# Optimization experiments

Hardware: AMD Instinct MI355X
Metric: run time of the kernel (lower is better)

## Reference

```python
import jax, jax.numpy as jnp
import numpy as np

B = 1024
D = 512
M = 65536          # num_memory
C = 4096           # num pseudo-label clusters (= labels.max()+1, fixed for jit)
TEMP = 0.05
EPS = 1e-6


def setup_inputs() -> dict:
    key = jax.random.key(0)
    k1, k2, k3, k4 = jax.random.split(key, 4)
    inputs = jax.random.normal(k1, (B, D), dtype=jnp.float32)
    indexes = jax.random.randint(k2, (B,), 0, M, dtype=jnp.int64)
    feats = jax.random.normal(k3, (M, D), dtype=jnp.float32)
    # memory bank stores L2-normalized features (see _update_feature)
    features = feats / jnp.linalg.norm(feats, axis=1, keepdims=True)
    labels = jax.random.randint(k4, (M,), 0, C, dtype=jnp.int64)
    return {"inputs": inputs, "indexes": indexes, "features": features, "labels": labels}


def reference(inputs, indexes, features, labels):
    # F.normalize(inputs, p=2, dim=1)
    x = inputs / jnp.linalg.norm(inputs, axis=1, keepdims=True)
    # HM.forward: inputs @ features.T, then / temp  -> sim over memory slots [B, M]
    sim = (x @ features.T) / TEMP
    # index_add over labels: per-cluster sum of sim columns  -> [C, B]
    sim_c = jax.ops.segment_sum(sim.T, labels, num_segments=C)
    nums = jax.ops.segment_sum(jnp.ones((M,), dtype=sim.dtype), labels, num_segments=C)  # [C]
    cluster_mask = (nums > 0).astype(sim.dtype)                     # [C]
    # mean within cluster; empty clusters divide by 1
    avg = sim_c / jnp.where(nums > 0, nums, 1.0)[:, None]           # [C, B]
    # masked_softmax over clusters, per sample
    vec = avg.T                                                     # [B, C]
    masked_exps = jnp.exp(vec) * cluster_mask[None, :]
    probs = masked_exps / (jnp.sum(masked_exps, axis=1, keepdims=True) + EPS)
    # F.nll_loss(log(probs + eps), targets) with targets = labels[indexes]
    targets = labels[indexes]                                       # [B]
    logp = jnp.log(probs + EPS)
    loss = -jnp.mean(logp[jnp.arange(B), targets])
    return loss
```

## Files before the change

kernel.cpp:

```cpp
#include <hip/hip_runtime.h>
#include <hip/hip_bf16.h>

#define NB 1024
#define ND 512
#define NM 65536
#define NC 4096
#define CAP 128

static constexpr float TEMP = 0.05f;
static constexpr float EPSF = 1e-6f;

typedef __attribute__((ext_vector_type(8))) short short8v;
typedef __attribute__((ext_vector_type(16))) float f32x16;

static __device__ __forceinline__ short f2bf(float f) {
    __hip_bfloat16 h = __float2bfloat16(f);
    return *reinterpret_cast<short*>(&h);
}

__global__ __launch_bounds__(128) void k_norm_init(const float* __restrict__ in,
                                                   const int* __restrict__ indexes,
                                                   const int* __restrict__ labels,
                                                   short* __restrict__ xnb,
                                                   int* __restrict__ tgt,
                                                   float* __restrict__ denom,
                                                   int* __restrict__ cnt) {
    int b = blockIdx.x;
    int t = threadIdx.x;
    const float4* row = reinterpret_cast<const float4*>(in + (size_t)b * ND);
    float4 v = row[t];
    float ss = v.x * v.x + v.y * v.y + v.z * v.z + v.w * v.w;
#pragma unroll
    for (int o = 32; o > 0; o >>= 1) ss += __shfl_down(ss, o);
    __shared__ float sw[2];
    int lane = t & 63, w = t >> 6;
    if (lane == 0) sw[w] = ss;
    __syncthreads();
    float inv = 1.0f / sqrtf(sw[0] + sw[1]);
    short4 o;
    o.x = f2bf(v.x * inv); o.y = f2bf(v.y * inv);
    o.z = f2bf(v.z * inv); o.w = f2bf(v.w * inv);
    reinterpret_cast<short4*>(xnb + (size_t)b * ND)[t] = o;
    if (b < 32) cnt[b * 128 + t] = 0;
    if (t == 0) {
        tgt[b] = labels[indexes[b]];
        denom[b] = 0.f;
    }
}

__global__ __launch_bounds__(256) void k_scatter(const int* __restrict__ labels,
                                                 int* __restrict__ cnt,
                                                 int* __restrict__ idx) {
    int m = blockIdx.x * 256 + threadIdx.x;
    int c = labels[m];
    int pos = atomicAdd(&cnt[c], 1);
    if (pos < CAP) idx[(size_t)c * CAP + pos] = m;
}

__global__ __launch_bounds__(128) void k_gather(const float* __restrict__ feats,
                                                const int* __restrict__ idx,
                                                const int* __restrict__ cnt,
                                                short* __restrict__ Gb) {
    int c = blockIdx.x;
    int t = threadIdx.x;
    int n = cnt[c];
    if (n > CAP) n = CAP;
    const int* bucket = idx + (size_t)c * CAP;
    const float4* F = reinterpret_cast<const float4*>(feats);
    float4 a0 = {0.f, 0.f, 0.f, 0.f}, a1 = {0.f, 0.f, 0.f, 0.f};
    float4 a2 = {0.f, 0.f, 0.f, 0.f}, a3 = {0.f, 0.f, 0.f, 0.f};
    int j = 0;
    for (; j + 3 < n; j += 4) {
        int m0 = bucket[j], m1 = bucket[j + 1];
        int m2 = bucket[j + 2], m3 = bucket[j + 3];
        float4 v0 = F[(size_t)m0 * 128 + t];
        float4 v1 = F[(size_t)m1 * 128 + t];
        float4 v2 = F[(size_t)m2 * 128 + t];
        float4 v3 = F[(size_t)m3 * 128 + t];
        a0.x += v0.x; a0.y += v0.y; a0.z += v0.z; a0.w += v0.w;
        a1.x += v1.x; a1.y += v1.y; a1.z += v1.z; a1.w += v1.w;
        a2.x += v2.x; a2.y += v2.y; a2.z += v2.z; a2.w += v2.w;
        a3.x += v3.x; a3.y += v3.y; a3.z += v3.z; a3.w += v3.w;
    }
    for (; j < n; ++j) {
        int m0 = bucket[j];
        float4 v0 = F[(size_t)m0 * 128 + t];
        a0.x += v0.x; a0.y += v0.y; a0.z += v0.z; a0.w += v0.w;
    }
    short4 o;
    o.x = f2bf(a0.x + a1.x + a2.x + a3.x);
    o.y = f2bf(a0.y + a1.y + a2.y + a3.y);
    o.z = f2bf(a0.z + a1.z + a2.z + a3.z);
    o.w = f2bf(a0.w + a1.w + a2.w + a3.w);
    reinterpret_cast<short4*>(Gb + (size_t)c * ND)[t] = o;
}

__global__ __launch_bounds__(256) void k_gemm_mfma(const short* __restrict__ A,
                                                   const short* __restrict__ Bm,
                                                   const int* __restrict__ cnt,
                                                   const int* __restrict__ tgt,
                                                   float* __restrict__ denom,
                                                   float* __restrict__ numer) {
    const int tid = threadIdx.x;
    const int w = tid >> 6;
    const int lane = tid & 63;
    const int ln = lane & 31;
    const int kg = lane >> 5;
    const int row0 = blockIdx.y * 128 + (w >> 1) * 64;
    const int col0 = blockIdx.x * 128 + (w & 1) * 64;

    f32x16 acc00 = {}, acc01 = {}, acc10 = {}, acc11 = {};
    const short* pa0 = A + (size_t)(row0 + ln) * ND + kg * 8;
    const short* pa1 = pa0 + 32 * ND;
    const short* pb0 = Bm + (size_t)(col0 + ln) * ND + kg * 8;
    const short* pb1 = pb0 + 32 * ND;
#pragma unroll 4
    for (int k0 = 0; k0 < ND; k0 += 16) {
        short8v a0 = *reinterpret_cast<const short8v*>(pa0 + k0);
        short8v a1 = *reinterpret_cast<const short8v*>(pa1 + k0);
        short8v b0 = *reinterpret_cast<const short8v*>(pb0 + k0);
        short8v b1 = *reinterpret_cast<const short8v*>(pb1 + k0);
        acc00 = __builtin_amdgcn_mfma_f32_32x32x16_bf16(a0, b0, acc00, 0, 0, 0);
        acc01 = __builtin_amdgcn_mfma_f32_32x32x16_bf16(a0, b1, acc01, 0, 0, 0);
        acc10 = __builtin_amdgcn_mfma_f32_32x32x16_bf16(a1, b0, acc10, 0, 0, 0);
        acc11 = __builtin_amdgcn_mfma_f32_32x32x16_bf16(a1, b1, acc11, 0, 0, 0);
    }
    int colA = col0 + ln;
    int colB = colA + 32;
    int nA = cnt[colA], nB = cnt[colB];
    float invA = 1.0f / (TEMP * (float)(nA > 0 ? nA : 1));
    float invB = 1.0f / (TEMP * (float)(nB > 0 ? nB : 1));
    float mA = (nA > 0) ? 1.f : 0.f;
    float mB = (nB > 0) ? 1.f : 0.f;
    int rbase = row0 + 4 * kg;
#pragma unroll
    for (int r = 0; r < 16; ++r) {
        int row = rbase + (r & 3) + 8 * (r >> 2);
        int rowH = row + 32;
        float v00 = acc00[r] * invA, v01 = acc01[r] * invB;
        float v10 = acc10[r] * invA, v11 = acc11[r] * invB;
        int t0 = tgt[row], t1 = tgt[rowH];
        if (t0 == colA) numer[row] = v00;
        if (t0 == colB) numer[row] = v01;
        if (t1 == colA) numer[rowH] = v10;
        if (t1 == colB) numer[rowH] = v11;
        float s0 = mA * __expf(v00) + mB * __expf(v01);
        float s1 = mA * __expf(v10) + mB * __expf(v11);
#pragma unroll
        for (int m = 1; m < 32; m <<= 1) {
            s0 += __shfl_xor(s0, m);
            s1 += __shfl_xor(s1, m);
        }
        if (ln == 0) {
            atomicAdd(&denom[row], s0);
            atomicAdd(&denom[rowH], s1);
        }
    }
}

__global__ __launch_bounds__(256) void k_final(const float* __restrict__ numer,
                                               const float* __restrict__ denom,
                                               float* __restrict__ out) {
    float s = 0.f;
    for (int i = threadIdx.x; i < NB; i += 256) {
        float p = __expf(numer[i]) / (denom[i] + EPSF);
        s += -logf(p + EPSF);
    }
#pragma unroll
    for (int o = 32; o > 0; o >>= 1) s += __shfl_down(s, o);
    __shared__ float sw[4];
    int lane = threadIdx.x & 63, w = threadIdx.x >> 6;
    if (lane == 0) sw[w] = s;
    __syncthreads();
    if (threadIdx.x == 0) out[0] = (sw[0] + sw[1] + sw[2] + sw[3]) / (float)NB;
}

extern "C" void kernel_launch(void* const* d_in, const int* in_sizes, int n_in,
                              void* d_out, int out_size, void* d_ws, size_t ws_size,
                              hipStream_t stream) {
    const float* inputs   = (const float*)d_in[0];
    const int*   indexes  = (const int*)d_in[1];
    const float* features = (const float*)d_in[2];
    const int*   labels   = (const int*)d_in[3];
    float* out = (float*)d_out;

    short* Gb     = (short*)d_ws;
    short* xnb    = Gb + (size_t)NC * ND;
    float* denom  = (float*)(xnb + (size_t)NB * ND);
    float* numer  = denom + NB;
    int*   tgt    = (int*)(numer + NB);
    int*   cnt    = tgt + NB;
    int*   idx    = cnt + NC;

    k_norm_init<<<NB, 128, 0, stream>>>(inputs, indexes, labels, xnb, tgt, denom, cnt);
    k_scatter<<<NM / 256, 256, 0, stream>>>(labels, cnt, idx);
    k_gather<<<NC, 128, 0, stream>>>(features, idx, cnt, Gb);
    dim3 g(NC / 128, NB / 128);
    k_gemm_mfma<<<g, 256, 0, stream>>>(xnb, Gb, cnt, tgt, denom, numer);
    k_final<<<1, 256, 0, stream>>>(numer, denom, out);
}
```

Before: 73.41 us.

## Fuse norm with scatter and fold final reduction into GEMM via completion flag

Buffer zeroing and target lookup move into a small init kernel. Input normalization is merged with the label scatter into one launch: four waves normalize rows while the other four do the atomic bucket scatter. The final loss reduction now runs inside the GEMM kernel: each block bumps a global counter, and block (0,0) spin-waits for all blocks before computing the loss. This cuts one kernel launch and its gap, at the cost of a spin-wait that assumes every GEMM block can be resident at the same time. The GEMM k-loop unroll is also raised from 4 to 8.

```diff
diff --git a/kernel.cpp b/kernel.cpp
--- a/kernel.cpp
+++ b/kernel.cpp
@@ -18,43 +18,47 @@
     return *reinterpret_cast<short*>(&h);
 }
 
-__global__ __launch_bounds__(128) void k_norm_init(const float* __restrict__ in,
-                                                   const int* __restrict__ indexes,
-                                                   const int* __restrict__ labels,
-                                                   short* __restrict__ xnb,
-                                                   int* __restrict__ tgt,
-                                                   float* __restrict__ denom,
-                                                   int* __restrict__ cnt) {
-    int b = blockIdx.x;
-    int t = threadIdx.x;
-    const float4* row = reinterpret_cast<const float4*>(in + (size_t)b * ND);
-    float4 v = row[t];
-    float ss = v.x * v.x + v.y * v.y + v.z * v.z + v.w * v.w;
-#pragma unroll
-    for (int o = 32; o > 0; o >>= 1) ss += __shfl_down(ss, o);
-    __shared__ float sw[2];
-    int lane = t & 63, w = t >> 6;
-    if (lane == 0) sw[w] = ss;
-    __syncthreads();
-    float inv = 1.0f / sqrtf(sw[0] + sw[1]);
-    short4 o;
-    o.x = f2bf(v.x * inv); o.y = f2bf(v.y * inv);
-    o.z = f2bf(v.z * inv); o.w = f2bf(v.w * inv);
-    reinterpret_cast<short4*>(xnb + (size_t)b * ND)[t] = o;
-    if (b < 32) cnt[b * 128 + t] = 0;
-    if (t == 0) {
-        tgt[b] = labels[indexes[b]];
-        denom[b] = 0.f;
-    }
-}
-
-__global__ __launch_bounds__(256) void k_scatter(const int* __restrict__ labels,
-                                                 int* __restrict__ cnt,
-                                                 int* __restrict__ idx) {
-    int m = blockIdx.x * 256 + threadIdx.x;
-    int c = labels[m];
-    int pos = atomicAdd(&cnt[c], 1);
-    if (pos < CAP) idx[(size_t)c * CAP + pos] = m;
+__global__ __launch_bounds__(256) void k_init(const int* __restrict__ indexes,
+                                              const int* __restrict__ labels,
+                                              int* __restrict__ cnt,
+                                              float* __restrict__ denom,
+                                              int* __restrict__ tgt,
+                                              int* __restrict__ flag) {
+    int i = blockIdx.x * 256 + threadIdx.x;
+    if (i < NC) cnt[i] = 0;
+    else if (i < NC + NB) denom[i - NC] = 0.f;
+    else if (i < NC + 2 * NB) { int b = i - NC - NB; tgt[b] = labels[indexes[b]]; }
+    else if (i == NC + 2 * NB) flag[0] = 0;
+}
+
+__global__ __launch_bounds__(512) void k_norm_scatter(const float* __restrict__ in,
+                                                      const int* __restrict__ labels,
+                                                      short* __restrict__ xnb,
+                                                      int* __restrict__ cnt,
+                                                      int* __restrict__ idx) {
+    const int b = blockIdx.x;
+    const int wid = threadIdx.x >> 6, l = threadIdx.x & 63;
+    if (wid < 4) {
+        int row = b * 4 + wid;
+        const float4* rp = reinterpret_cast<const float4*>(in + (size_t)row * ND) + l * 2;
+        float4 v0 = rp[0], v1 = rp[1];
+        float ss = v0.x * v0.x + v0.y * v0.y + v0.z * v0.z + v0.w * v0.w
+                 + v1.x * v1.x + v1.y * v1.y + v1.z * v1.z + v1.w * v1.w;
+#pragma unroll
+        for (int m = 1; m < 64; m <<= 1) ss += __shfl_xor(ss, m);
+        float inv = 1.0f / sqrtf(ss);
+        short8v o;
+        o[0] = f2bf(v0.x * inv); o[1] = f2bf(v0.y * inv);
+        o[2] = f2bf(v0.z * inv); o[3] = f2bf(v0.w * inv);
+        o[4] = f2bf(v1.x * inv); o[5] = f2bf(v1.y * inv);
+        o[6] = f2bf(v1.z * inv); o[7] = f2bf(v1.w * inv);
+        *reinterpret_cast<short8v*>(xnb + (size_t)row * ND + l * 8) = o;
+    } else {
+        int m = b * 256 + (threadIdx.x - 256);
+        int c = labels[m];
+        int pos = atomicAdd(&cnt[c], 1);
+        if (pos < CAP) idx[(size_t)c * CAP + pos] = m;
+    }
 }
 
 __global__ __launch_bounds__(128) void k_gather(const float* __restrict__ feats,
@@ -95,12 +99,14 @@
     reinterpret_cast<short4*>(Gb + (size_t)c * ND)[t] = o;
 }
 
-__global__ __launch_bounds__(256) void k_gemm_mfma(const short* __restrict__ A,
-                                                   const short* __restrict__ Bm,
-                                                   const int* __restrict__ cnt,
-                                                   const int* __restrict__ tgt,
-                                                   float* __restrict__ denom,
-                                                   float* __restrict__ numer) {
+__global__ __launch_bounds__(256) void k_gemm_final(const short* __restrict__ A,
+                                                    const short* __restrict__ Bm,
+                                                    const int* __restrict__ cnt,
+                                                    const int* __restrict__ tgt,
+                                                    float* __restrict__ denom,
+                                                    float* __restrict__ numer,
+                                                    int* __restrict__ flag,
+                                                    float* __restrict__ out) {
     const int tid = threadIdx.x;
     const int w = tid >> 6;
     const int lane = tid & 63;
@@ -114,7 +120,7 @@
     const short* pa1 = pa0 + 32 * ND;
     const short* pb0 = Bm + (size_t)(col0 + ln) * ND + kg * 8;
     const short* pb1 = pb0 + 32 * ND;
-#pragma unroll 4
+#pragma unroll 8
     for (int k0 = 0; k0 < ND; k0 += 16) {
         short8v a0 = *reinterpret_cast<const short8v*>(pa0 + k0);
         short8v a1 = *reinterpret_cast<const short8v*>(pa1 + k0);
@@ -156,23 +162,30 @@
             atomicAdd(&denom[rowH], s1);
         }
     }
-}
-
-__global__ __launch_bounds__(256) void k_final(const float* __restrict__ numer,
-                                               const float* __restrict__ denom,
-                                               float* __restrict__ out) {
+
+    __syncthreads();
+    if (tid == 0) {
+        __threadfence();
+        atomicAdd(flag, 1);
+    }
+    if (blockIdx.x != 0 || blockIdx.y != 0) return;
+
+    if (tid == 0) {
+        while (atomicAdd(flag, 0) < 256) __builtin_amdgcn_s_sleep(8);
+        __threadfence();
+    }
+    __syncthreads();
     float s = 0.f;
-    for (int i = threadIdx.x; i < NB; i += 256) {
+    for (int i = tid; i < NB; i += 256) {
         float p = __expf(numer[i]) / (denom[i] + EPSF);
         s += -logf(p + EPSF);
     }
 #pragma unroll
     for (int o = 32; o > 0; o >>= 1) s += __shfl_down(s, o);
     __shared__ float sw[4];
-    int lane = threadIdx.x & 63, w = threadIdx.x >> 6;
     if (lane == 0) sw[w] = s;
     __syncthreads();
-    if (threadIdx.x == 0) out[0] = (sw[0] + sw[1] + sw[2] + sw[3]) / (float)NB;
+    if (tid == 0) out[0] = (sw[0] + sw[1] + sw[2] + sw[3]) / (float)NB;
 }
 
 extern "C" void kernel_launch(void* const* d_in, const int* in_sizes, int n_in,
@@ -189,13 +202,13 @@
     float* denom  = (float*)(xnb + (size_t)NB * ND);
     float* numer  = denom + NB;
     int*   tgt    = (int*)(numer + NB);
-    int*   cnt    = tgt + NB;
+    int*   flag   = tgt + NB;
+    int*   cnt    = flag + 64;
     int*   idx    = cnt + NC;
 
-    k_norm_init<<<NB, 128, 0, stream>>>(inputs, indexes, labels, xnb, tgt, denom, cnt);
-    k_scatter<<<NM / 256, 256, 0, stream>>>(labels, cnt, idx);
+    k_init<<<25, 256, 0, stream>>>(indexes, labels, cnt, denom, tgt, flag);
+    k_norm_scatter<<<NB / 4, 512, 0, stream>>>(inputs, labels, xnb, cnt, idx);
     k_gather<<<NC, 128, 0, stream>>>(features, idx, cnt, Gb);
     dim3 g(NC / 128, NB / 128);
-    k_gemm_mfma<<<g, 256, 0, stream>>>(xnb, Gb, cnt, tgt, denom, numer);
-    k_final<<<1, 256, 0, stream>>>(numer, denom, out);
-}
+    k_gemm_final<<<g, 256, 0, stream>>>(xnb, Gb, cnt, tgt, denom, numer, flag, out);
+}
```

Result: slower. 75.62 us (+3.0%).
